# Kernel optimization log

Hardware: AMD Instinct MI355X
Metric: run time of the kernel (lower is better)

The kernel has to match this reference:

```python
import jax, jax.numpy as jnp
import numpy as np

# LeNet-5 custom connectivity between S2 (6 ch) and C3 (16 ch): MAP[i, o] = 1 if input ch i feeds output ch o
MAP_INFO = np.array([
    [1, 0, 0, 0, 1, 1, 1, 0, 0, 1, 1, 1, 1, 0, 1, 1],
    [1, 1, 0, 0, 0, 1, 1, 1, 0, 0, 1, 1, 1, 1, 0, 1],
    [1, 1, 1, 0, 0, 0, 1, 1, 1, 0, 0, 1, 0, 1, 1, 1],
    [0, 1, 1, 1, 0, 0, 1, 1, 1, 1, 0, 0, 1, 0, 1, 1],
    [0, 0, 1, 1, 1, 0, 0, 1, 1, 1, 1, 0, 1, 1, 0, 1],
    [0, 0, 0, 1, 1, 1, 0, 0, 1, 1, 1, 1, 0, 1, 1, 1],
], dtype=np.float32)  # [6, 16]

SCALE = 1.7159
SLOPE = 2.0 / 3.0


def _conv(x, w):
    # x: [B, Cin, H, W], w: [Cout, Cin, kh, kw], VALID padding, stride 1
    return jax.lax.conv_general_dilated(
        x, w, window_strides=(1, 1), padding='VALID',
        dimension_numbers=('NCHW', 'OIHW', 'NCHW'))


def _subsample(x, w, b):
    # 2x2 average pool then per-channel affine (trainable scale/bias)
    B, C, H, W = x.shape
    p = x.reshape(B, C, H // 2, 2, W // 2, 2).mean(axis=(3, 5))
    return p * w[None, :, None, None] + b[None, :, None, None]


def _act(x):
    return SCALE * jnp.tanh(SLOPE * x)


def setup_inputs() -> dict:
    key = jax.random.key(0)
    ks = jax.random.split(key, 16)
    B = 8192

    def unif(k, shape, fan_in):
        return (jax.random.uniform(k, shape, dtype=jnp.float32) * 4.8 - 2.4) / fan_in

    x = jax.random.normal(ks[0], (B, 1, 32, 32), dtype=jnp.float32)
    c1_w = unif(ks[1], (6, 1, 5, 5), 25 * 1)
    c1_b = jax.random.uniform(ks[2], (6,), dtype=jnp.float32) * 0.1
    s2_w = unif(ks[3], (6,), 4)
    s2_b = jax.random.uniform(ks[4], (6,), dtype=jnp.float32)
    c3_w = unif(ks[5], (16, 6, 5, 5), 25 * 6)
    c3_b = jax.random.uniform(ks[6], (16,), dtype=jnp.float32) * 0.1
    s4_w = unif(ks[7], (16,), 4)
    s4_b = jax.random.uniform(ks[8], (16,), dtype=jnp.float32)
    c5_w = unif(ks[9], (120, 16, 5, 5), 25 * 16)
    c5_b = jax.random.uniform(ks[10], (120,), dtype=jnp.float32) * 0.1
    f6_w = unif(ks[11], (84, 120), 120)
    f6_b = jax.random.uniform(ks[12], (84,), dtype=jnp.float32) * 0.1
    rbf_w = jax.random.uniform(ks[13], (84, 10), dtype=jnp.float32)
    return dict(x=x, c1_w=c1_w, c1_b=c1_b, s2_w=s2_w, s2_b=s2_b,
                c3_w=c3_w, c3_b=c3_b, s4_w=s4_w, s4_b=s4_b,
                c5_w=c5_w, c5_b=c5_b, f6_w=f6_w, f6_b=f6_b, rbf_w=rbf_w)


def reference(x, c1_w, c1_b, s2_w, s2_b, c3_w, c3_b, s4_w, s4_b,
              c5_w, c5_b, f6_w, f6_b, rbf_w):
    # C1: 1->6 conv5, replicate padding 2 -> [B,6,32,32]
    xp = jnp.pad(x, ((0, 0), (0, 0), (2, 2), (2, 2)), mode='edge')
    h = _conv(xp, c1_w) + c1_b[None, :, None, None]
    # S2 + squashing act -> [B,6,16,16]
    h = _act(_subsample(h, s2_w, s2_b))
    # C3: sparse-connectivity conv expressed as dense conv with masked weights -> [B,16,12,12]
    mask = jnp.asarray(MAP_INFO.T)[:, :, None, None]  # [16,6,1,1]
    h = _conv(h, c3_w * mask) + c3_b[None, :, None, None]
    # S4 + act -> [B,16,6,6]
    h = _act(_subsample(h, s4_w, s4_b))
    # C5: 16->120 conv5 -> [B,120,1,1]
    h = _conv(h, c5_w) + c5_b[None, :, None, None]
    h = h.reshape(-1, 120)
    # F6 + act -> [B,84]
    h = _act(h @ f6_w.T + f6_b)
    # RBF output: squared euclidean distance to class prototypes -> [B,10]
    out = jnp.sum((h[:, :, None] - rbf_w[None, :, :]) ** 2, axis=1)
    return out
```

## Files before the change

### kernel.cpp

```cpp
#include <hip/hip_runtime.h>
#include <math.h>

typedef _Float16 h16;
typedef h16  h8v __attribute__((ext_vector_type(8)));
typedef h16  h4v __attribute__((ext_vector_type(4)));
typedef h16  h2v __attribute__((ext_vector_type(2)));
typedef float f4v __attribute__((ext_vector_type(4)));
typedef unsigned int u32;

#define WS_B1   0
#define WS_B3   8
#define WS_KB1  24
#define WS_W3H  408
#define WS_W5H  2712
#define WS_F6H  29336
#define WS_RBFT 35480

#define L_B3    0
#define L_C5B   64
#define L_F6B   544
#define L_S2H   880
#define L_A5    880
#define L_HB    880
#define L_RBF   6512
#define L_XPAD  14704
#define L_S4    14704
#define L_A6    14704
#define L_GUARD 19888
#define LDS_TOTAL 20080

__device__ const unsigned char MASK16[16] = {7,14,28,56,49,35,15,30,60,57,51,39,27,54,45,63};

__device__ __forceinline__ float squash(float x) {
    float E = __expf(1.33333333f * x);
    return 1.7159f - 3.4318f * __builtin_amdgcn_rcpf(1.0f + E);
}

__device__ __forceinline__ void slot_to_uv(int c, int& u, int& v) {
    u = -1; v = 0;
    if (c < 32) {
        int q = c >> 3, j = c & 7;
        if (j < 6)       { u = q;     v = j; }
        else if (q == 2) { u = 4;     v = j - 6; }
        else if (q == 3) { u = 5;     v = j - 6; }
    } else {
        int cc = c - 32, q = cc >> 2, j = cc & 3;
        if (q == 0)      { u = 4;     v = 2 + j; }
        else if (q == 1) { u = 5;     v = 2 + j; }
    }
}

__global__ __launch_bounds__(256) void prep_kernel(
    const float* __restrict__ c1_w, const float* __restrict__ c1_b,
    const float* __restrict__ s2_w, const float* __restrict__ s2_b,
    const float* __restrict__ c3_w, const float* __restrict__ c3_b,
    const float* __restrict__ s4_w, const float* __restrict__ s4_b,
    const float* __restrict__ c5_w, const float* __restrict__ f6_w,
    const float* __restrict__ rbf_w,
    float* __restrict__ ws)
{
    const int gid = blockIdx.x * 256 + threadIdx.x;
    const int gstr = gridDim.x * 256;
    if (gid < 6)  ws[WS_B1 + gid] = s2_w[gid] * c1_b[gid] + s2_b[gid];
    if (gid < 16) ws[WS_B3 + gid] = s4_w[gid] * c3_b[gid] + s4_b[gid];
    h16* KB1 = (h16*)(ws + WS_KB1);
    for (int idx = gid; idx < 768; idx += gstr) {
        int n = idx / 48, c = idx - n * 48;
        int u, v; slot_to_uv(c, u, v);
        float val = 0.f;
        if (n < 6 && u >= 0) {
            float s = 0.f;
            #pragma unroll
            for (int dy = 0; dy < 2; ++dy)
                #pragma unroll
                for (int dx = 0; dx < 2; ++dx) {
                    int ky = u - dy, kx = v - dx;
                    if (ky >= 0 && ky < 5 && kx >= 0 && kx < 5)
                        s += c1_w[(n * 5 + ky) * 5 + kx];
                }
            val = 0.25f * s * s2_w[n];
        }
        KB1[idx] = (h16)val;
    }
    h16* W3H = (h16*)(ws + WS_W3H);
    for (int idx = gid; idx < 4608; idx += gstr) {
        int i = idx / 768, r = idx - i * 768;
        int n = r / 48, c = r - n * 48;
        int u, v; slot_to_uv(c, u, v);
        float val = 0.f;
        if (u >= 0) {
            float s = 0.f;
            #pragma unroll
            for (int dy = 0; dy < 2; ++dy)
                #pragma unroll
                for (int dx = 0; dx < 2; ++dx) {
                    int ky = u - dy, kx = v - dx;
                    if (ky >= 0 && ky < 5 && kx >= 0 && kx < 5)
                        s += c3_w[((n * 6 + i) * 5 + ky) * 5 + kx];
                }
            val = ((MASK16[n] >> i) & 1) ? 0.25f * s4_w[n] * s : 0.f;
        }
        W3H[idx] = (h16)val;
    }
    h16* W5H = (h16*)(ws + WS_W5H);
    for (int idx = gid; idx < 53248; idx += gstr) {
        int kb = idx >> 12, rr = idx & 4095;
        int n = rr >> 5, k = rr & 31;
        int kg = kb * 32 + k;
        int i = kg / 26, r = kg - i * 26;
        float val = (n < 120 && r < 25) ? c5_w[n * 400 + i * 25 + r] : 0.f;
        W5H[idx] = (h16)val;
    }
    h16* F6H = (h16*)(ws + WS_F6H);
    for (int idx = gid; idx < 12288; idx += gstr) {
        int n = idx >> 7, k = idx & 127;
        float val = (n < 84 && k < 120) ? f6_w[n * 120 + k] : 0.f;
        F6H[idx] = (h16)val;
    }
    for (int idx = gid; idx < 840; idx += gstr) {
        int k = idx / 10, c = idx - k * 10;
        ws[WS_RBFT + c * 84 + k] = rbf_w[idx];
    }
}

__global__ __launch_bounds__(256, 8) void lenet_kernel(
    const float* __restrict__ x,
    const float* __restrict__ c5_b, const float* __restrict__ f6_b,
    const float* __restrict__ ws,
    float* __restrict__ out)
{
    __shared__ __align__(16) char smem[LDS_TOTAL];
    float* s_b3  = (float*)(smem + L_B3);
    float* s_c5b = (float*)(smem + L_C5B);
    float* s_f6b = (float*)(smem + L_F6B);
    float* s_rbf = (float*)(smem + L_RBF);
    h16*  XPAD   = (h16*)(smem + L_XPAD);
    h16*  S2H    = (h16*)(smem + L_S2H);
    h16*  S4     = (h16*)(smem + L_S4);
    h16*  A5     = (h16*)(smem + L_A5);
    h16*  A6     = (h16*)(smem + L_A6);
    float* HB    = (float*)(smem + L_HB);

    const int tid  = threadIdx.x;
    const int wave = __builtin_amdgcn_readfirstlane(tid >> 6);
    const int lane = tid & 63;
    const int quad = lane >> 4;
    const int lr   = lane & 15;

    if (tid < 16)  s_b3[tid] = ws[WS_B3 + tid];
    if (tid < 120) s_c5b[tid] = c5_b[tid];
    if (tid < 84)  s_f6b[tid] = f6_b[tid];
    if (tid < 48)  ((u32*)(smem + L_GUARD))[tid] = 0u;
    const float* xb = x + (size_t)blockIdx.x * 4096;
    const h16* KB1 = (const h16*)(ws + WS_KB1);
    h8v w1a = *(const h8v*)(KB1 + lr * 48 + quad * 8);
    h4v w1b = *(const h4v*)(KB1 + lr * 48 + 32 + quad * 4);
    float b1v = ws[WS_B1 + (lr < 6 ? lr : 0)];

    auto stageA = [&](int s) {
        #pragma unroll
        for (int k = 0; k < 2; ++k) {
            int idx = tid + k * 256;
            int im = idx >> 8;
            int r  = (idx >> 3) & 31;
            int c4 = idx & 7;
            float4 v = *(const float4*)(xb + (2 * s + im) * 1024 + r * 32 + c4 * 4);
            h2v p0; p0.x = (h16)v.x; p0.y = (h16)v.y;
            h2v p1; p1.x = (h16)v.z; p1.y = (h16)v.w;
            h16* d = XPAD + im * 1296 + (r + 2) * 36 + (4 * c4 + 2);
            *(h2v*)(d)     = p0;
            *(h2v*)(d + 2) = p1;
        }
        #pragma unroll
        for (int k = 0; k < 3; ++k) {
            int e = tid + k * 256;
            if (e < 544) {
                int im = (e >= 272) ? 1 : 0;
                int h = e - 272 * im;
                int u, v;
                if (h < 144) { int q = h / 36; u = (q < 2) ? q : 32 + q; v = h - q * 36; }
                else { int g = h - 144; u = 2 + (g >> 2); int q = g & 3; v = (q < 2) ? q : 32 + q; }
                int sr = min(max(u - 2, 0), 31), sc = min(max(v - 2, 0), 31);
                XPAD[im * 1296 + u * 36 + v] = (h16)xb[(2 * s + im) * 1024 + sr * 32 + sc];
            }
        }
    };

    auto stageB = [&](int s) {
        const h16* bp = XPAD + (wave >> 1) * 1296 + (wave & 1) * 576 + 2 * lr;
        h16* s2base = S2H + (s * 2 + (wave >> 1)) * 1728 + lr * 288 + (wave & 1) * 144 + quad * 4;
        #pragma unroll
        for (int tt = 0; tt < 8; ++tt) {
            const u32* bq = (const u32*)bp + quad * 18;
            union { u32 u[4]; h8v h; } av;
            av.u[0] = bq[0];  av.u[1] = bq[1];
            av.u[2] = bq[2];  av.u[3] = bq[36];
            f4v acc = {b1v, b1v, b1v, b1v};
            acc = __builtin_amdgcn_mfma_f32_16x16x32_f16(av.h, w1a, acc, 0, 0, 0);
            union { u32 u[2]; h4v h; } av2;
            av2.u[0] = bq[73]; av2.u[1] = bq[74];
            acc = __builtin_amdgcn_mfma_f32_16x16x16f16(av2.h, w1b, acc, 0, 0, 0);
            if (lr < 6) {
                h2v q0; q0.x = (h16)squash(acc[0]); q0.y = (h16)squash(acc[1]);
                h2v q1; q1.x = (h16)squash(acc[2]); q1.y = (h16)squash(acc[3]);
                *(h2v*)(s2base + tt * 18)     = q0;
                *(h2v*)(s2base + tt * 18 + 2) = q1;
            }
            bp += 72;
        }
    };

    stageA(0);
    __syncthreads();
    stageB(0);
    __syncthreads();
    stageA(1);
    __syncthreads();
    stageB(1);
    __syncthreads();

    f4v cacc0, cacc1, cacc2;
    const bool w0 = (wave == 0);
    {
        const h16* W3H = (const h16*)(ws + WS_W3H);
        int baseh0, baseh1, baseh2;
        {
            int m0 = wave * 16 + lr;
            int i0 = m0 / 36, p0 = m0 - i0 * 36;
            baseh0 = i0 * 1728 + (2 * (p0 / 6)) * 18 + 2 * (p0 % 6);
            int m1 = (wave + 4) * 16 + lr;
            int i1 = m1 / 36, p1 = m1 - i1 * 36;
            baseh1 = i1 * 1728 + (2 * (p1 / 6)) * 18 + 2 * (p1 % 6);
            int m2 = 128 + lr;
            int i2 = m2 / 36, p2 = m2 - i2 * 36;
            baseh2 = i2 * 1728 + (2 * (p2 / 6)) * 18 + 2 * (p2 % 6);
        }
        float b3v = s_b3[lr];
        f4v cinit = {b3v, b3v, b3v, b3v};
        cacc0 = cinit; cacc1 = cinit; cacc2 = cinit;
        #pragma unroll
        for (int i = 0; i < 6; ++i) {
            const h16* bbase = W3H + i * 768 + lr * 48;
            h8v w3a = *(const h8v*)(bbase + quad * 8);
            h4v w3b = *(const h4v*)(bbase + 32 + quad * 4);
            {
                const u32* cq = (const u32*)(S2H + baseh0 + i * 288) + quad * 9;
                union { u32 u[4]; h8v h; } av;
                av.u[0] = cq[0];  av.u[1] = cq[1];
                av.u[2] = cq[2];  av.u[3] = cq[18];
                cacc0 = __builtin_amdgcn_mfma_f32_16x16x32_f16(av.h, w3a, cacc0, 0, 0, 0);
                union { u32 u[2]; h4v h; } av2;
                av2.u[0] = cq[37]; av2.u[1] = cq[38];
                cacc0 = __builtin_amdgcn_mfma_f32_16x16x16f16(av2.h, w3b, cacc0, 0, 0, 0);
            }
            {
                const u32* cq = (const u32*)(S2H + baseh1 + i * 288) + quad * 9;
                union { u32 u[4]; h8v h; } av;
                av.u[0] = cq[0];  av.u[1] = cq[1];
                av.u[2] = cq[2];  av.u[3] = cq[18];
                cacc1 = __builtin_amdgcn_mfma_f32_16x16x32_f16(av.h, w3a, cacc1, 0, 0, 0);
                union { u32 u[2]; h4v h; } av2;
                av2.u[0] = cq[37]; av2.u[1] = cq[38];
                cacc1 = __builtin_amdgcn_mfma_f32_16x16x16f16(av2.h, w3b, cacc1, 0, 0, 0);
            }
            if (w0) {
                const u32* cq = (const u32*)(S2H + baseh2 + i * 288) + quad * 9;
                union { u32 u[4]; h8v h; } av;
                av.u[0] = cq[0];  av.u[1] = cq[1];
                av.u[2] = cq[2];  av.u[3] = cq[18];
                cacc2 = __builtin_amdgcn_mfma_f32_16x16x32_f16(av.h, w3a, cacc2, 0, 0, 0);
                union { u32 u[2]; h4v h; } av2;
                av2.u[0] = cq[37]; av2.u[1] = cq[38];
                cacc2 = __builtin_amdgcn_mfma_f32_16x16x16f16(av2.h, w3b, cacc2, 0, 0, 0);
            }
        }
    }

    const h16* W5H = (const h16*)(ws + WS_W5H);
    h8v bf0c = *(const h8v*)(W5H + (wave * 32 + lr) * 32 + quad * 8);
    h8v bf1c = *(const h8v*)(W5H + (wave * 32 + 16 + lr) * 32 + quad * 8);

    {
        #pragma unroll
        for (int r = 0; r < 4; ++r) {
            int m = wave * 16 + quad * 4 + r;
            int img = m / 36, pos = m - img * 36;
            S4[img * 672 + lr * 42 + pos] = (h16)squash(cacc0[r]);
        }
        #pragma unroll
        for (int r = 0; r < 4; ++r) {
            int m = (wave + 4) * 16 + quad * 4 + r;
            int img = m / 36, pos = m - img * 36;
            S4[img * 672 + lr * 42 + pos] = (h16)squash(cacc1[r]);
        }
        if (w0) {
            #pragma unroll
            for (int r = 0; r < 4; ++r) {
                int m = 128 + quad * 4 + r;
                int img = m / 36, pos = m - img * 36;
                S4[img * 672 + lr * 42 + pos] = (h16)squash(cacc2[r]);
            }
        }
    }
    __syncthreads();

    {
        int m = tid >> 4, i = tid & 15;
        int img = m >> 2, q = m & 3, qy = q >> 1, qx = q & 1;
        const h16* s4b = S4 + img * 672 + i * 42 + qy * 6 + qx;
        u32* dst = (u32*)(A5 + m * 424 + i * 26);
        #pragma unroll
        for (int w = 0; w < 12; ++w) {
            int k0 = 2 * w, k1 = 2 * w + 1;
            union { h2v h; u32 u; } p;
            p.h.x = s4b[(k0 / 5) * 6 + (k0 % 5)];
            p.h.y = s4b[(k1 / 5) * 6 + (k1 % 5)];
            dst[w] = p.u;
        }
        {
            union { h2v h; u32 u; } p;
            p.h.x = s4b[28];
            p.h.y = (h16)0.f;
            dst[12] = p.u;
        }
    }
    __syncthreads();

    {
        h8v af0c = *(const h8v*)(A5 + lr * 424 + quad * 8);
        float c5b0 = s_c5b[wave * 32 + lr];
        float c5b1 = s_c5b[wave * 32 + 16 + lr];
        f4v dacc0 = {c5b0, c5b0, c5b0, c5b0};
        f4v dacc1 = {c5b1, c5b1, c5b1, c5b1};
        #pragma unroll
        for (int i = 0; i < 13; ++i) {
            h8v bf0n, bf1n, af0n;
            if (i < 12) {
                bf0n = *(const h8v*)(W5H + (i + 1) * 4096 + (wave * 32 + lr) * 32 + quad * 8);
                bf1n = *(const h8v*)(W5H + (i + 1) * 4096 + (wave * 32 + 16 + lr) * 32 + quad * 8);
                af0n = *(const h8v*)(A5 + lr * 424 + (i + 1) * 32 + quad * 8);
            }
            dacc0 = __builtin_amdgcn_mfma_f32_16x16x32_f16(af0c, bf0c, dacc0, 0, 0, 0);
            dacc1 = __builtin_amdgcn_mfma_f32_16x16x32_f16(af0c, bf1c, dacc1, 0, 0, 0);
            if (i < 12) { bf0c = bf0n; bf1c = bf1n; af0c = af0n; }
        }
        if (tid < 64) {
            int m = tid >> 2, j = tid & 3;
            *(u32*)(A6 + m * 136 + 120 + 2 * j) = 0u;
        }
        {
            int n0 = wave * 32 + lr;
            if (n0 < 120) {
                int tt = n0 / 30, cb = (n0 - tt * 30) * 4;
                #pragma unroll
                for (int r = 0; r < 4; ++r) {
                    int m = quad * 4 + r;
                    A6[((m >> 2) * 4 + tt) * 136 + cb + (m & 3)] = (h16)dacc0[r];
                }
            }
            int n1 = wave * 32 + 16 + lr;
            if (n1 < 120) {
                int tt = n1 / 30, cb = (n1 - tt * 30) * 4;
                #pragma unroll
                for (int r = 0; r < 4; ++r) {
                    int m = quad * 4 + r;
                    A6[((m >> 2) * 4 + tt) * 136 + cb + (m & 3)] = (h16)dacc1[r];
                }
            }
        }
    }

    const h16* F6H = (const h16*)(ws + WS_F6H);
    const int wv2 = (wave < 2) ? wave + 4 : wave;
    h8v eb0c = *(const h8v*)(F6H + (wave * 16 + lr) * 128 + quad * 8);
    h8v eb1c = *(const h8v*)(F6H + (wv2 * 16 + lr) * 128 + quad * 8);
    float4 rv = {0.f, 0.f, 0.f, 0.f};
    if (tid < 210) rv = *(const float4*)(ws + WS_RBFT + tid * 4);
    __syncthreads();

    if (tid < 210) *(float4*)(s_rbf + tid * 4) = rv;

    {
        h8v a8c = *(const h8v*)(A6 + lr * 136 + quad * 8);
        float f60 = s_f6b[wave * 16 + lr];
        f4v eacc0 = {f60, f60, f60, f60};
        f4v eacc1 = {};
        const bool w2 = (wave < 2);
        if (w2) {
            int n1 = (wave + 4) * 16 + lr;
            float f61 = (n1 < 84) ? s_f6b[n1] : 0.f;
            eacc1[0] = f61; eacc1[1] = f61; eacc1[2] = f61; eacc1[3] = f61;
        }
        #pragma unroll
        for (int kc = 0; kc < 4; ++kc) {
            h8v eb0n, eb1n, a8n;
            if (kc < 3) {
                eb0n = *(const h8v*)(F6H + (wave * 16 + lr) * 128 + (kc + 1) * 32 + quad * 8);
                eb1n = *(const h8v*)(F6H + (wv2 * 16 + lr) * 128 + (kc + 1) * 32 + quad * 8);
                a8n  = *(const h8v*)(A6 + lr * 136 + (kc + 1) * 32 + quad * 8);
            }
            eacc0 = __builtin_amdgcn_mfma_f32_16x16x32_f16(a8c, eb0c, eacc0, 0, 0, 0);
            if (w2)
                eacc1 = __builtin_amdgcn_mfma_f32_16x16x32_f16(a8c, eb1c, eacc1, 0, 0, 0);
            if (kc < 3) { eb0c = eb0n; eb1c = eb1n; a8c = a8n; }
        }
        {
            int n = wave * 16 + lr;
            #pragma unroll
            for (int r = 0; r < 4; ++r) {
                int m = quad * 4 + r;
                HB[m * 88 + n] = squash(eacc0[r]);
            }
        }
        if (w2) {
            int n = (wave + 4) * 16 + lr;
            if (n < 84) {
                #pragma unroll
                for (int r = 0; r < 4; ++r) {
                    int m = quad * 4 + r;
                    HB[m * 88 + n] = squash(eacc1[r]);
                }
            }
        }
    }
    __syncthreads();

    if (tid < 160) {
        int m = tid / 10, cls = tid - m * 10;
        const float4* hr = (const float4*)(HB + m * 88);
        const float4* pr = (const float4*)(s_rbf + cls * 84);
        float a = 0.f;
        #pragma unroll
        for (int u = 0; u < 21; ++u) {
            float4 hv = hr[u], pv = pr[u];
            float dx = hv.x - pv.x, dy = hv.y - pv.y;
            float dz = hv.z - pv.z, dw = hv.w - pv.w;
            a += dx * dx + dy * dy + dz * dz + dw * dw;
        }
        out[(size_t)blockIdx.x * 160 + tid] = a;
    }
}

extern "C" void kernel_launch(void* const* d_in, const int* in_sizes, int n_in,
                              void* d_out, int out_size, void* d_ws, size_t ws_size,
                              hipStream_t stream) {
    (void)n_in; (void)out_size; (void)ws_size;
    const float* x     = (const float*)d_in[0];
    const float* c1_w  = (const float*)d_in[1];
    const float* c1_b  = (const float*)d_in[2];
    const float* s2_w  = (const float*)d_in[3];
    const float* s2_b  = (const float*)d_in[4];
    const float* c3_w  = (const float*)d_in[5];
    const float* c3_b  = (const float*)d_in[6];
    const float* s4_w  = (const float*)d_in[7];
    const float* s4_b  = (const float*)d_in[8];
    const float* c5_w  = (const float*)d_in[9];
    const float* c5_b  = (const float*)d_in[10];
    const float* f6_w  = (const float*)d_in[11];
    const float* f6_b  = (const float*)d_in[12];
    const float* rbf_w = (const float*)d_in[13];
    float* out = (float*)d_out;
    float* ws  = (float*)d_ws;

    const int B = in_sizes[0] / 1024;

    prep_kernel<<<256, 256, 0, stream>>>(c1_w, c1_b, s2_w, s2_b, c3_w, c3_b,
                                         s4_w, s4_b, c5_w, f6_w, rbf_w, ws);
    lenet_kernel<<<B / 4, 256, 0, stream>>>(x, c5_b, f6_b, ws, out);
}
```

Measured before the change: 133.4 us.

## Compute RBF distances via MFMA expansion ||h||²-2h·p+||p||²

Replaces the per-thread fp32 squared-distance loop over 84 features with an algebraic expansion done on matrix cores. Prototypes are pre-scaled by -2 and stored as fp16, their squared norms are precomputed in the prep kernel, and H·Hᵀ plus H·Pᵀ are computed with MFMA. The diagonal of H·Hᵀ is then pulled out with lane shuffles. This removes the fp32 RBF table staging in LDS, but adds fp16 rounding of activations and prototypes plus cancellation error in the expanded form.

```diff
diff --git a/kernel.cpp b/kernel.cpp
--- a/kernel.cpp
+++ b/kernel.cpp
@@ -14,15 +14,15 @@
 #define WS_W3H  408
 #define WS_W5H  2712
 #define WS_F6H  29336
-#define WS_RBFT 35480
+#define WS_RBFH 35480
+#define WS_PSQ  36248
 
 #define L_B3    0
 #define L_C5B   64
 #define L_F6B   544
 #define L_S2H   880
 #define L_A5    880
-#define L_HB    880
-#define L_RBF   6512
+#define L_HBH   880
 #define L_XPAD  14704
 #define L_S4    14704
 #define L_A6    14704
@@ -117,9 +117,19 @@
         float val = (n < 84 && k < 120) ? f6_w[n * 120 + k] : 0.f;
         F6H[idx] = (h16)val;
     }
-    for (int idx = gid; idx < 840; idx += gstr) {
-        int k = idx / 10, c = idx - k * 10;
-        ws[WS_RBFT + c * 84 + k] = rbf_w[idx];
+    h16* RBFH = (h16*)(ws + WS_RBFH);
+    for (int idx = gid; idx < 1536; idx += gstr) {
+        int n = idx / 96, k = idx - n * 96;
+        float val = (n < 10 && k < 84) ? -2.f * rbf_w[k * 10 + n] : 0.f;
+        RBFH[idx] = (h16)val;
+    }
+    if (gid < 10) {
+        float s = 0.f;
+        for (int k = 0; k < 84; ++k) {
+            float pv = (float)(h16)rbf_w[k * 10 + gid];
+            s += pv * pv;
+        }
+        ws[WS_PSQ + gid] = s;
     }
 }
 
@@ -133,13 +143,12 @@
     float* s_b3  = (float*)(smem + L_B3);
     float* s_c5b = (float*)(smem + L_C5B);
     float* s_f6b = (float*)(smem + L_F6B);
-    float* s_rbf = (float*)(smem + L_RBF);
     h16*  XPAD   = (h16*)(smem + L_XPAD);
     h16*  S2H    = (h16*)(smem + L_S2H);
     h16*  S4     = (h16*)(smem + L_S4);
     h16*  A5     = (h16*)(smem + L_A5);
     h16*  A6     = (h16*)(smem + L_A6);
-    float* HB    = (float*)(smem + L_HB);
+    h16*  HBH    = (h16*)(smem + L_HBH);
 
     const int tid  = threadIdx.x;
     const int wave = __builtin_amdgcn_readfirstlane(tid >> 6);
@@ -156,6 +165,7 @@
     h8v w1a = *(const h8v*)(KB1 + lr * 48 + quad * 8);
     h4v w1b = *(const h4v*)(KB1 + lr * 48 + 32 + quad * 4);
     float b1v = ws[WS_B1 + (lr < 6 ? lr : 0)];
+    float psqv = ws[WS_PSQ + (lr < 10 ? lr : 0)];
 
     auto stageA = [&](int s) {
         #pragma unroll
@@ -374,11 +384,12 @@
     const int wv2 = (wave < 2) ? wave + 4 : wave;
     h8v eb0c = *(const h8v*)(F6H + (wave * 16 + lr) * 128 + quad * 8);
     h8v eb1c = *(const h8v*)(F6H + (wv2 * 16 + lr) * 128 + quad * 8);
-    float4 rv = {0.f, 0.f, 0.f, 0.f};
-    if (tid < 210) rv = *(const float4*)(ws + WS_RBFT + tid * 4);
-    __syncthreads();
-
-    if (tid < 210) *(float4*)(s_rbf + tid * 4) = rv;
+    __syncthreads();
+
+    if (tid < 96) {
+        int m = tid / 6, j = tid - m * 6;
+        ((u32*)HBH)[m * 48 + 42 + j] = 0u;
+    }
 
     {
         h8v a8c = *(const h8v*)(A6 + lr * 136 + quad * 8);
@@ -409,7 +420,7 @@
             #pragma unroll
             for (int r = 0; r < 4; ++r) {
                 int m = quad * 4 + r;
-                HB[m * 88 + n] = squash(eacc0[r]);
+                HBH[m * 96 + n] = (h16)squash(eacc0[r]);
             }
         }
         if (w2) {
@@ -418,26 +429,36 @@
                 #pragma unroll
                 for (int r = 0; r < 4; ++r) {
                     int m = quad * 4 + r;
-                    HB[m * 88 + n] = squash(eacc1[r]);
+                    HBH[m * 96 + n] = (h16)squash(eacc1[r]);
                 }
             }
         }
     }
     __syncthreads();
 
-    if (tid < 160) {
-        int m = tid / 10, cls = tid - m * 10;
-        const float4* hr = (const float4*)(HB + m * 88);
-        const float4* pr = (const float4*)(s_rbf + cls * 84);
-        float a = 0.f;
-        #pragma unroll
-        for (int u = 0; u < 21; ++u) {
-            float4 hv = hr[u], pv = pr[u];
-            float dx = hv.x - pv.x, dy = hv.y - pv.y;
-            float dz = hv.z - pv.z, dw = hv.w - pv.w;
-            a += dx * dx + dy * dy + dz * dz + dw * dw;
-        }
-        out[(size_t)blockIdx.x * 160 + tid] = a;
+    if (w0) {
+        const h16* RBFH = (const h16*)(ws + WS_RBFH);
+        h8v gb0 = *(const h8v*)(RBFH + lr * 96 + quad * 8);
+        h8v gb1 = *(const h8v*)(RBFH + lr * 96 + 32 + quad * 8);
+        h8v gb2 = *(const h8v*)(RBFH + lr * 96 + 64 + quad * 8);
+        h8v ga0 = *(const h8v*)(HBH + lr * 96 + quad * 8);
+        h8v ga1 = *(const h8v*)(HBH + lr * 96 + 32 + quad * 8);
+        h8v ga2 = *(const h8v*)(HBH + lr * 96 + 64 + quad * 8);
+        f4v hh = {};
+        hh = __builtin_amdgcn_mfma_f32_16x16x32_f16(ga0, ga0, hh, 0, 0, 0);
+        hh = __builtin_amdgcn_mfma_f32_16x16x32_f16(ga1, ga1, hh, 0, 0, 0);
+        hh = __builtin_amdgcn_mfma_f32_16x16x32_f16(ga2, ga2, hh, 0, 0, 0);
+        f4v d2 = {psqv, psqv, psqv, psqv};
+        d2 = __builtin_amdgcn_mfma_f32_16x16x32_f16(ga0, gb0, d2, 0, 0, 0);
+        d2 = __builtin_amdgcn_mfma_f32_16x16x32_f16(ga1, gb1, d2, 0, 0, 0);
+        d2 = __builtin_amdgcn_mfma_f32_16x16x32_f16(ga2, gb2, d2, 0, 0, 0);
+        float* ob = out + (size_t)blockIdx.x * 160;
+        #pragma unroll
+        for (int r = 0; r < 4; ++r) {
+            float hsq = __shfl(hh[r], quad * 20 + r);
+            if (lr < 10)
+                ob[(quad * 4 + r) * 10 + lr] = hsq + d2[r];
+        }
     }
 }
 
```

After: 132.6 us. No clear change (-0.6%).
